# Optimization experiments

Hardware: AMD Instinct MI355X
Metric: run time of the kernel (lower is better)

The kernel has to match this reference:

```python
import jax, jax.numpy as jnp
import numpy as np

B, D, M = 16384, 512, 16

def setup_inputs() -> dict:
    key = jax.random.key(0)
    k1, k2, k3 = jax.random.split(key, 3)
    z = jax.random.normal(k1, (B, D), dtype=jnp.float32)
    # Psi: n_dynamics small [D,D] operators (orthogonal-init in torch; random here)
    Psi = jax.random.normal(k2, (M, D, D), dtype=jnp.float32) * 0.001
    gate_tokens = jax.random.normal(k3, (M, D), dtype=jnp.float32) * (1.0 / np.sqrt(D))
    t = jnp.zeros((1,), dtype=jnp.float32)  # unused by forward, kept for signature parity
    return {"t": t, "z": z, "Psi": Psi, "gate_tokens": gate_tokens}

def reference(t, z, Psi, gate_tokens):
    # scores[b,m,e] = (z @ Psi_m)[b,e]  -- batched small GEMM over M dynamics
    scores = jnp.einsum('bd,mde->bme', z, Psi)
    # gate logits and sparse-soft gates: relu(2*sigmoid(logits) - 1)
    logits = jnp.einsum('bme,me->bm', scores, gate_tokens)
    gates = jax.nn.relu(2.0 * jax.nn.sigmoid(logits) - 1.0)
    # dz[b,e] = sum_m gates[b,m] * scores[b,m,e]
    dz = jnp.einsum('bm,bme->be', gates, scores)
    return dz
```

## Files before the change

kernel.cpp:

```cpp
#include <hip/hip_runtime.h>
#include <hip/hip_bf16.h>

#define B_N 16384
#define D_N 512
#define M_N 16
#define NT  128

typedef __attribute__((ext_vector_type(4))) float  f32x4;
typedef __attribute__((ext_vector_type(8))) short  s16x8;

__device__ __forceinline__ short bf16_of(float f) {
  union { float f; unsigned u; } v; v.f = f;
  unsigned r = v.u + 0x7fffu + ((v.u >> 16) & 1u);
  return (short)(r >> 16);
}
__device__ __forceinline__ float f32_of_bf16(unsigned short u) {
  union { unsigned u; float f; } v; v.u = ((unsigned)u) << 16; return v.f;
}
__device__ __forceinline__ void gload_lds16(const void* g, void* l) {
  __builtin_amdgcn_global_load_lds(
      (const __attribute__((address_space(1))) unsigned*)g,
      (__attribute__((address_space(3))) unsigned*)l, 16, 0, 0);
}

#define MFMA_ACC(d, x, y) d = __builtin_amdgcn_mfma_f32_16x16x32_bf16(x, y, d, 0, 0, 0)

__global__ void k_trw(const float* __restrict__ Psi, const float* __restrict__ gt,
                      short* __restrict__ Psib, float* __restrict__ wT) {
  int m = blockIdx.y, d0 = blockIdx.x << 6;
  __shared__ float tile[64][65];
  __shared__ float gs[D_N];
  int t = threadIdx.x;
  for (int i = t; i < D_N; i += 256) gs[i] = gt[m * D_N + i];
  int r = t >> 2, q = t & 3;
  float wacc = 0.f;
  const float* src = Psi + (size_t)m * D_N * D_N;
  short* dst = Psib + (size_t)m * D_N * D_N;
  for (int e0 = 0; e0 < D_N; e0 += 64) {
    __syncthreads();
    #pragma unroll
    for (int j = 0; j < 4; ++j) {
      int idx = t + (j << 8);
      int rr = idx >> 4, c4 = idx & 15;
      *(f32x4*)&tile[rr][c4 * 4] = *(const f32x4*)(src + (size_t)(d0 + rr) * D_N + e0 + c4 * 4);
    }
    __syncthreads();
    #pragma unroll
    for (int k = 0; k < 16; ++k) wacc += tile[r][q * 16 + k] * gs[e0 + q * 16 + k];
    #pragma unroll
    for (int it = 0; it < 2; ++it) {
      int idx = t + (it << 8);
      int el = idx >> 3, jb = idx & 7;
      int e = e0 + el;
      s16x8 o;
      #pragma unroll
      for (int k = 0; k < 8; ++k) o[k] = bf16_of(tile[jb * 8 + k][el]);
      int db = jb ^ (e & 7);
      *(s16x8*)(dst + (size_t)e * D_N + d0 + db * 8) = o;
    }
  }
  wacc += __shfl_xor(wacc, 1);
  wacc += __shfl_xor(wacc, 2);
  if (q == 0) wT[(d0 + r) * M_N + m] = wacc;
}

__global__ void k_gz(const float* __restrict__ z, const float* __restrict__ wT,
                     short* __restrict__ zb, unsigned short* __restrict__ gatesb) {
  __shared__ float zs[16][D_N];
  int t = threadIdx.x;
  size_t b0 = (size_t)blockIdx.x * 16;
  #pragma unroll
  for (int j = 0; j < 8; ++j) {
    int idx = t + (j << 8);
    int r = idx >> 7, c4 = idx & 127;
    *(f32x4*)&zs[r][c4 * 4] = *(const f32x4*)(z + (b0 + r) * D_N + c4 * 4);
  }
  __syncthreads();
  int r = t >> 4, m = t & 15;
  float s0 = 0.f, s1 = 0.f, s2 = 0.f, s3 = 0.f;
  #pragma unroll 4
  for (int e = 0; e < D_N; e += 4) {
    s0 += zs[r][e + 0] * wT[(e + 0) * M_N + m];
    s1 += zs[r][e + 1] * wT[(e + 1) * M_N + m];
    s2 += zs[r][e + 2] * wT[(e + 2) * M_N + m];
    s3 += zs[r][e + 3] * wT[(e + 3) * M_N + m];
  }
  float s = (s0 + s1) + (s2 + s3);
  float sig = 1.f / (1.f + expf(-s));
  gatesb[(b0 + r) * M_N + m] = (unsigned short)bf16_of(fmaxf(2.f * sig - 1.f, 0.f));
  #pragma unroll
  for (int j = 0; j < 4; ++j) {
    int idx = t + (j << 8);
    int rr = idx >> 6, blk = idx & 63;
    int chunk = blk >> 3, ib = blk & 7;
    int sb = ib ^ (rr & 7);
    const float* sp = &zs[rr][chunk * 64 + sb * 8];
    s16x8 o;
    #pragma unroll
    for (int k = 0; k < 8; ++k) o[k] = bf16_of(sp[k]);
    *(s16x8*)(zb + (b0 + rr) * D_N + blk * 8) = o;
  }
}

__global__ __launch_bounds__(512, 2) void k_gemm(
    const char* __restrict__ zb, const unsigned short* __restrict__ gatesb,
    const char* __restrict__ pb, float* __restrict__ dz) {
  __shared__ __align__(128) char smem[3 * 49152 + 8192];
  char* gates_lds = smem + 3 * 49152;

  const int tid = threadIdx.x;
  const int lane = tid & 63;
  const int wid = tid >> 6;
  const int wr = wid >> 1, wc = wid & 1;
  const int bid = blockIdx.x;
  const int xcd = bid & 7;
  const int g8  = bid >> 3;
  const int bcol = g8 & 3;
  const int brow = xcd * 8 + (g8 >> 2);

  {
    s16x8 gv = *(const s16x8*)(gatesb + ((size_t)brow << 12) + ((size_t)tid << 3));
    unsigned short* gl = (unsigned short*)gates_lds;
    int row = tid >> 1, mbase = (tid & 1) << 3;
    #pragma unroll
    for (int k = 0; k < 8; ++k)
      gl[(mbase + k) * 256 + row] = (unsigned short)gv[k];
  }
  asm volatile("s_waitcnt vmcnt(0)" ::: "memory");

  const int rsub = lane >> 3, cbyte = (lane & 7) << 4;
  const size_t srcA0 = ((size_t)(brow * 256 + wid * 8 + rsub) << 10) + cbyte;
  const size_t srcB0 = ((size_t)(bcol * 128 + wid * 8 + rsub) << 10) + cbyte;
  const int dstA0 = wid << 10;
  const int dstB0 = 32768 + (wid << 10);

  auto stageA = [&](char* buf, int t, int j) {
    gload_lds16(zb + srcA0 + (size_t)(j << 16) + ((t & 7) << 7),
                buf + dstA0 + (j << 13));
  };
  auto stageB = [&](char* buf, int t, int j) {
    gload_lds16(pb + (((size_t)(t >> 3)) << 19) + srcB0 + (size_t)(j << 16) + ((t & 7) << 7),
                buf + dstB0 + (j << 13));
  };

  const int lrow = lane & 15;
  const int swz = (lrow & 7) << 4;
  const int offA0 = ((wr * 64 + lrow) << 7) + (((lane >> 4) << 4) ^ swz);
  const int offB0 = 32768 + ((wc * 64 + lrow) << 7) + (((lane >> 4) << 4) ^ swz);

  f32x4 acc[4][4] = {};
  f32x4 accm[4][4] = {};

  char* p0 = smem;
  char* p1 = smem + 49152;
  char* p2 = smem + 2 * 49152;

  #pragma unroll
  for (int j = 0; j < 4; ++j) stageA(p0, 0, j);
  stageB(p0, 0, 0); stageB(p0, 0, 1);
  #pragma unroll
  for (int j = 0; j < 4; ++j) stageA(p1, 1, j);
  stageB(p1, 1, 0); stageB(p1, 1, 1);
  asm volatile("s_waitcnt vmcnt(6) lgkmcnt(0)" ::: "memory");
  __builtin_amdgcn_s_barrier();

  for (int t = 0; t < NT; ++t) {
    const bool st = (t + 2) < NT;
    s16x8 a[4][2], b[4][2];

    #pragma unroll
    for (int ks = 0; ks < 2; ++ks) {
      a[0][ks] = *(const s16x8*)(p0 + ((offA0 +    0) ^ (ks << 6)));
      a[1][ks] = *(const s16x8*)(p0 + ((offA0 + 2048) ^ (ks << 6)));
      #pragma unroll
      for (int nf = 0; nf < 4; ++nf)
        b[nf][ks] = *(const s16x8*)(p0 + ((offB0 + nf * 2048) ^ (ks << 6)));
    }
    if (st) { stageA(p2, t + 2, 0); stageA(p2, t + 2, 1); stageA(p2, t + 2, 2); }
    __builtin_amdgcn_s_barrier();
    __builtin_amdgcn_s_setprio(1);
    #pragma unroll
    for (int ks = 0; ks < 2; ++ks) {
      MFMA_ACC(accm[0][0], a[0][ks], b[0][ks]);
      MFMA_ACC(accm[0][1], a[0][ks], b[1][ks]);
      MFMA_ACC(accm[1][0], a[1][ks], b[0][ks]);
      MFMA_ACC(accm[1][1], a[1][ks], b[1][ks]);
      MFMA_ACC(accm[0][2], a[0][ks], b[2][ks]);
      MFMA_ACC(accm[0][3], a[0][ks], b[3][ks]);
      MFMA_ACC(accm[1][2], a[1][ks], b[2][ks]);
      MFMA_ACC(accm[1][3], a[1][ks], b[3][ks]);
    }
    __builtin_amdgcn_s_setprio(0);
    __builtin_amdgcn_s_barrier();

    #pragma unroll
    for (int ks = 0; ks < 2; ++ks) {
      a[2][ks] = *(const s16x8*)(p0 + ((offA0 + 2 * 2048) ^ (ks << 6)));
      a[3][ks] = *(const s16x8*)(p0 + ((offA0 + 3 * 2048) ^ (ks << 6)));
    }
    if (st) { stageA(p2, t + 2, 3); stageB(p2, t + 2, 0); stageB(p2, t + 2, 1); }
    __builtin_amdgcn_s_barrier();
    __builtin_amdgcn_s_setprio(1);
    #pragma unroll
    for (int ks = 0; ks < 2; ++ks) {
      MFMA_ACC(accm[2][0], a[2][ks], b[0][ks]);
      MFMA_ACC(accm[2][1], a[2][ks], b[1][ks]);
      MFMA_ACC(accm[3][0], a[3][ks], b[0][ks]);
      MFMA_ACC(accm[3][1], a[3][ks], b[1][ks]);
      MFMA_ACC(accm[2][2], a[2][ks], b[2][ks]);
      MFMA_ACC(accm[2][3], a[2][ks], b[3][ks]);
      MFMA_ACC(accm[3][2], a[3][ks], b[2][ks]);
      MFMA_ACC(accm[3][3], a[3][ks], b[3][ks]);
    }
    __builtin_amdgcn_s_setprio(0);

    if ((t & 7) == 7) {
      int m = t >> 3;
      const unsigned short* gl = (const unsigned short*)gates_lds;
      #pragma unroll
      for (int mf = 0; mf < 4; ++mf) {
        int rl = wr * 64 + mf * 16 + ((lane >> 4) << 2);
        #pragma unroll
        for (int j = 0; j < 4; ++j) {
          float g = f32_of_bf16(gl[m * 256 + rl + j]);
          #pragma unroll
          for (int nf = 0; nf < 4; ++nf)
            acc[mf][nf][j] += g * accm[mf][nf][j];
        }
      }
      #pragma unroll
      for (int mf = 0; mf < 4; ++mf)
        #pragma unroll
        for (int nf = 0; nf < 4; ++nf)
          accm[mf][nf] = f32x4{0.f, 0.f, 0.f, 0.f};
    }

    if (st) asm volatile("s_waitcnt vmcnt(6)" ::: "memory");
    else    asm volatile("s_waitcnt vmcnt(0)" ::: "memory");
    __builtin_amdgcn_s_barrier();
    char* tmp = p0; p0 = p1; p1 = p2; p2 = tmp;
  }

  #pragma unroll
  for (int mf = 0; mf < 4; ++mf) {
    #pragma unroll
    for (int nf = 0; nf < 4; ++nf) {
      int col = bcol * 128 + wc * 64 + nf * 16 + (lane & 15);
      size_t rbase = (size_t)brow * 256 + wr * 64 + mf * 16 + ((lane >> 4) << 2);
      #pragma unroll
      for (int j = 0; j < 4; ++j)
        dz[(rbase + j) * D_N + col] = acc[mf][nf][j];
    }
  }
}

extern "C" void kernel_launch(void* const* d_in, const int* in_sizes, int n_in,
                              void* d_out, int out_size, void* d_ws, size_t ws_size,
                              hipStream_t stream) {
  const float* z   = (const float*)d_in[1];
  const float* Psi = (const float*)d_in[2];
  const float* gt  = (const float*)d_in[3];
  float* dz = (float*)d_out;

  float* wT = (float*)d_ws;
  unsigned short* gatesb = (unsigned short*)((char*)d_ws + 32768);
  short* Psib = (short*)((char*)d_ws + 32768 + 524288);
  short* zb16 = Psib + (size_t)M_N * D_N * D_N;

  k_trw <<<dim3(8, M_N), dim3(256), 0, stream>>>(Psi, gt, Psib, wT);
  k_gz  <<<dim3(B_N / 16), dim3(256), 0, stream>>>(z, wT, zb16, gatesb);
  k_gemm<<<dim3(256), dim3(512), 0, stream>>>((const char*)zb16, gatesb,
                                              (const char*)Psib, dz);
}
```

Baseline: 177.2 us.

## Reorder GEMM loop to keep A fragments in registers across dynamics

```diff
diff --git a/kernel.cpp b/kernel.cpp
--- a/kernel.cpp
+++ b/kernel.cpp
@@ -4,7 +4,6 @@
 #define B_N 16384
 #define D_N 512
 #define M_N 16
-#define NT  128
 
 typedef __attribute__((ext_vector_type(4))) float  f32x4;
 typedef __attribute__((ext_vector_type(8))) short  s16x8;
@@ -105,151 +104,138 @@
 __global__ __launch_bounds__(512, 2) void k_gemm(
     const char* __restrict__ zb, const unsigned short* __restrict__ gatesb,
     const char* __restrict__ pb, float* __restrict__ dz) {
-  __shared__ __align__(128) char smem[3 * 49152 + 8192];
-  char* gates_lds = smem + 3 * 49152;
+  __shared__ __align__(128) char smem[139264];
 
   const int tid = threadIdx.x;
   const int lane = tid & 63;
   const int wid = tid >> 6;
-  const int wr = wid >> 1, wc = wid & 1;
+  const int wr = wid >> 1;
+  const int wc = wid & 1;
   const int bid = blockIdx.x;
   const int xcd = bid & 7;
-  const int g8  = bid >> 3;
+  const int g8 = bid >> 3;
   const int bcol = g8 & 3;
   const int brow = xcd * 8 + (g8 >> 2);
 
   {
     s16x8 gv = *(const s16x8*)(gatesb + ((size_t)brow << 12) + ((size_t)tid << 3));
-    unsigned short* gl = (unsigned short*)gates_lds;
+    unsigned short* gl = (unsigned short*)(smem + 131072);
     int row = tid >> 1, mbase = (tid & 1) << 3;
     #pragma unroll
     for (int k = 0; k < 8; ++k)
       gl[(mbase + k) * 256 + row] = (unsigned short)gv[k];
   }
-  asm volatile("s_waitcnt vmcnt(0)" ::: "memory");
 
   const int rsub = lane >> 3, cbyte = (lane & 7) << 4;
-  const size_t srcA0 = ((size_t)(brow * 256 + wid * 8 + rsub) << 10) + cbyte;
-  const size_t srcB0 = ((size_t)(bcol * 128 + wid * 8 + rsub) << 10) + cbyte;
-  const int dstA0 = wid << 10;
-  const int dstB0 = 32768 + (wid << 10);
-
-  auto stageA = [&](char* buf, int t, int j) {
-    gload_lds16(zb + srcA0 + (size_t)(j << 16) + ((t & 7) << 7),
-                buf + dstA0 + (j << 13));
+
+  auto stageA = [&](int ab, int dc) {
+    #pragma unroll
+    for (int j = 0; j < 4; ++j) {
+      const char* g = zb + (((size_t)(brow * 256 + wid * 8 + j * 64 + rsub)) << 10)
+                      + (dc << 7) + cbyte;
+      gload_lds16(g, smem + ab * 32768 + (wid << 10) + (j << 13));
+    }
   };
-  auto stageB = [&](char* buf, int t, int j) {
-    gload_lds16(pb + (((size_t)(t >> 3)) << 19) + srcB0 + (size_t)(j << 16) + ((t & 7) << 7),
-                buf + dstB0 + (j << 13));
+  auto stageB = [&](int s) {
+    int m = s & 15, dc = s >> 4, q = s & 3;
+    #pragma unroll
+    for (int j = 0; j < 2; ++j) {
+      const char* g = pb + (((size_t)(m * 512 + bcol * 128 + wid * 8 + j * 64 + rsub)) << 10)
+                      + (dc << 7) + cbyte;
+      gload_lds16(g, smem + 65536 + q * 16384 + (wid << 10) + (j << 13));
+    }
   };
 
   const int lrow = lane & 15;
   const int swz = (lrow & 7) << 4;
-  const int offA0 = ((wr * 64 + lrow) << 7) + (((lane >> 4) << 4) ^ swz);
-  const int offB0 = 32768 + ((wc * 64 + lrow) << 7) + (((lane >> 4) << 4) ^ swz);
+  const int kq16 = (((lane >> 4) << 4)) ^ swz;
+  const int offY = ((wr * 64 + lrow) << 7) + kq16;
+  const int offX = ((wc * 64 + lrow) << 7) + kq16;
 
   f32x4 acc[4][4] = {};
   f32x4 accm[4][4] = {};
-
-  char* p0 = smem;
-  char* p1 = smem + 49152;
-  char* p2 = smem + 2 * 49152;
-
-  #pragma unroll
-  for (int j = 0; j < 4; ++j) stageA(p0, 0, j);
-  stageB(p0, 0, 0); stageB(p0, 0, 1);
-  #pragma unroll
-  for (int j = 0; j < 4; ++j) stageA(p1, 1, j);
-  stageB(p1, 1, 0); stageB(p1, 1, 1);
-  asm volatile("s_waitcnt vmcnt(6) lgkmcnt(0)" ::: "memory");
+  s16x8 areg[4][2];
+  s16x8 bx[4], by[4];
+
+  stageA(0, 0);
+  stageB(0); stageB(1); stageB(2);
+  asm volatile("s_waitcnt vmcnt(0) lgkmcnt(0)" ::: "memory");
   __builtin_amdgcn_s_barrier();
-
-  for (int t = 0; t < NT; ++t) {
-    const bool st = (t + 2) < NT;
-    s16x8 a[4][2], b[4][2];
-
-    #pragma unroll
-    for (int ks = 0; ks < 2; ++ks) {
-      a[0][ks] = *(const s16x8*)(p0 + ((offA0 +    0) ^ (ks << 6)));
-      a[1][ks] = *(const s16x8*)(p0 + ((offA0 + 2048) ^ (ks << 6)));
-      #pragma unroll
-      for (int nf = 0; nf < 4; ++nf)
-        b[nf][ks] = *(const s16x8*)(p0 + ((offB0 + nf * 2048) ^ (ks << 6)));
-    }
-    if (st) { stageA(p2, t + 2, 0); stageA(p2, t + 2, 1); stageA(p2, t + 2, 2); }
+  #pragma unroll
+  for (int i = 0; i < 4; ++i)
+    bx[i] = *(const s16x8*)(smem + 65536 + (offX + i * 2048));
+
+  for (int s = 0; s < 128; ++s) {
+    const int m = s & 15, dc = s >> 4;
+    const char* bbase_cur = smem + 65536 + (s & 3) * 16384;
+    const char* bbase_nxt = smem + 65536 + ((s + 1) & 3) * 16384;
+
+    if (m == 0) {
+      const char* abase = smem + (dc & 1) * 32768;
+      #pragma unroll
+      for (int j = 0; j < 4; ++j) {
+        areg[j][0] = *(const s16x8*)(abase + (offY + j * 2048));
+        areg[j][1] = *(const s16x8*)(abase + ((offY + j * 2048) ^ 64));
+      }
+    }
+    #pragma unroll
+    for (int i = 0; i < 4; ++i)
+      by[i] = *(const s16x8*)(bbase_cur + ((offX + i * 2048) ^ 64));
+    if (s + 3 < 128) stageB(s + 3);
+    if (m == 11 && dc < 7) stageA((dc & 1) ^ 1, dc + 1);
+    float gj[4];
+    {
+      const unsigned short* gl = (const unsigned short*)(smem + 131072);
+      #pragma unroll
+      for (int j = 0; j < 4; ++j)
+        gj[j] = f32_of_bf16(gl[m * 256 + wr * 64 + j * 16 + lrow]);
+    }
+    __builtin_amdgcn_s_setprio(1);
+    #pragma unroll
+    for (int i = 0; i < 4; ++i)
+      #pragma unroll
+      for (int j = 0; j < 4; ++j)
+        MFMA_ACC(accm[i][j], bx[i], areg[j][0]);
+    __builtin_amdgcn_s_setprio(0);
+
+    if (s < 127) {
+      #pragma unroll
+      for (int i = 0; i < 4; ++i)
+        bx[i] = *(const s16x8*)(bbase_nxt + (offX + i * 2048));
+    }
+    __builtin_amdgcn_s_setprio(1);
+    #pragma unroll
+    for (int i = 0; i < 4; ++i)
+      #pragma unroll
+      for (int j = 0; j < 4; ++j)
+        MFMA_ACC(accm[i][j], by[i], areg[j][1]);
+    __builtin_amdgcn_s_setprio(0);
+    #pragma unroll
+    for (int i = 0; i < 4; ++i)
+      #pragma unroll
+      for (int j = 0; j < 4; ++j) {
+        #pragma unroll
+        for (int jj = 0; jj < 4; ++jj)
+          acc[i][j][jj] += gj[j] * accm[i][j][jj];
+        accm[i][j] = f32x4{0.f, 0.f, 0.f, 0.f};
+      }
+
+    if (dc < 7 && (m == 11 || m == 12))
+      asm volatile("s_waitcnt vmcnt(6)" ::: "memory");
+    else if (s >= 125)
+      asm volatile("s_waitcnt vmcnt(0)" ::: "memory");
+    else
+      asm volatile("s_waitcnt vmcnt(2)" ::: "memory");
     __builtin_amdgcn_s_barrier();
-    __builtin_amdgcn_s_setprio(1);
-    #pragma unroll
-    for (int ks = 0; ks < 2; ++ks) {
-      MFMA_ACC(accm[0][0], a[0][ks], b[0][ks]);
-      MFMA_ACC(accm[0][1], a[0][ks], b[1][ks]);
-      MFMA_ACC(accm[1][0], a[1][ks], b[0][ks]);
-      MFMA_ACC(accm[1][1], a[1][ks], b[1][ks]);
-      MFMA_ACC(accm[0][2], a[0][ks], b[2][ks]);
-      MFMA_ACC(accm[0][3], a[0][ks], b[3][ks]);
-      MFMA_ACC(accm[1][2], a[1][ks], b[2][ks]);
-      MFMA_ACC(accm[1][3], a[1][ks], b[3][ks]);
-    }
-    __builtin_amdgcn_s_setprio(0);
-    __builtin_amdgcn_s_barrier();
-
-    #pragma unroll
-    for (int ks = 0; ks < 2; ++ks) {
-      a[2][ks] = *(const s16x8*)(p0 + ((offA0 + 2 * 2048) ^ (ks << 6)));
-      a[3][ks] = *(const s16x8*)(p0 + ((offA0 + 3 * 2048) ^ (ks << 6)));
-    }
-    if (st) { stageA(p2, t + 2, 3); stageB(p2, t + 2, 0); stageB(p2, t + 2, 1); }
-    __builtin_amdgcn_s_barrier();
-    __builtin_amdgcn_s_setprio(1);
-    #pragma unroll
-    for (int ks = 0; ks < 2; ++ks) {
-      MFMA_ACC(accm[2][0], a[2][ks], b[0][ks]);
-      MFMA_ACC(accm[2][1], a[2][ks], b[1][ks]);
-      MFMA_ACC(accm[3][0], a[3][ks], b[0][ks]);
-      MFMA_ACC(accm[3][1], a[3][ks], b[1][ks]);
-      MFMA_ACC(accm[2][2], a[2][ks], b[2][ks]);
-      MFMA_ACC(accm[2][3], a[2][ks], b[3][ks]);
-      MFMA_ACC(accm[3][2], a[3][ks], b[2][ks]);
-      MFMA_ACC(accm[3][3], a[3][ks], b[3][ks]);
-    }
-    __builtin_amdgcn_s_setprio(0);
-
-    if ((t & 7) == 7) {
-      int m = t >> 3;
-      const unsigned short* gl = (const unsigned short*)gates_lds;
-      #pragma unroll
-      for (int mf = 0; mf < 4; ++mf) {
-        int rl = wr * 64 + mf * 16 + ((lane >> 4) << 2);
-        #pragma unroll
-        for (int j = 0; j < 4; ++j) {
-          float g = f32_of_bf16(gl[m * 256 + rl + j]);
-          #pragma unroll
-          for (int nf = 0; nf < 4; ++nf)
-            acc[mf][nf][j] += g * accm[mf][nf][j];
-        }
-      }
-      #pragma unroll
-      for (int mf = 0; mf < 4; ++mf)
-        #pragma unroll
-        for (int nf = 0; nf < 4; ++nf)
-          accm[mf][nf] = f32x4{0.f, 0.f, 0.f, 0.f};
-    }
-
-    if (st) asm volatile("s_waitcnt vmcnt(6)" ::: "memory");
-    else    asm volatile("s_waitcnt vmcnt(0)" ::: "memory");
-    __builtin_amdgcn_s_barrier();
-    char* tmp = p0; p0 = p1; p1 = p2; p2 = tmp;
-  }
-
-  #pragma unroll
-  for (int mf = 0; mf < 4; ++mf) {
-    #pragma unroll
-    for (int nf = 0; nf < 4; ++nf) {
-      int col = bcol * 128 + wc * 64 + nf * 16 + (lane & 15);
-      size_t rbase = (size_t)brow * 256 + wr * 64 + mf * 16 + ((lane >> 4) << 2);
-      #pragma unroll
-      for (int j = 0; j < 4; ++j)
-        dz[(rbase + j) * D_N + col] = acc[mf][nf][j];
+  }
+
+  #pragma unroll
+  for (int i = 0; i < 4; ++i) {
+    int e = bcol * 128 + wc * 64 + i * 16 + ((lane >> 4) << 2);
+    #pragma unroll
+    for (int j = 0; j < 4; ++j) {
+      size_t b = (size_t)brow * 256 + wr * 64 + j * 16 + lrow;
+      *(f32x4*)(dz + b * D_N + e) = acc[i][j];
     }
   }
 }
```

Measured after the change: 157.6 us. 1.12x faster.
